# Kernel optimization log

Hardware: AMD Instinct MI355X
Metric: run time of the kernel (lower is better)

Reference implementation:

```python
import jax, jax.numpy as jnp
import numpy as np

B, T, IN = 64, 366, 24
H1, H2, HM, PEN, C = 1024, 2048, 2048, 1024, 21


def setup_inputs() -> dict:
    key = jax.random.key(0)
    ks = jax.random.split(key, 20)
    s = 0.02
    inp = {
        'x': jax.random.normal(ks[0], (B, T, IN), jnp.float32),
        'cultivar_label': jax.random.randint(ks[1], (B, 1), 0, C, jnp.int64),
        'W1': jax.random.normal(ks[2], (H1, IN), jnp.float32) * s,
        'b1': jnp.zeros((H1,), jnp.float32),
        'W2': jax.random.normal(ks[3], (H2, H1), jnp.float32) * s,
        'b2': jnp.zeros((H2,), jnp.float32),
        'W_ih': jax.random.normal(ks[4], (3 * HM, H2), jnp.float32) * s,
        'W_hh': jax.random.normal(ks[5], (3 * HM, HM), jnp.float32) * s,
        'b_ih': jnp.zeros((3 * HM,), jnp.float32),
        'b_hh': jnp.zeros((3 * HM,), jnp.float32),
        'W3': jax.random.normal(ks[6], (PEN, HM), jnp.float32) * s,
        'b3': jnp.zeros((PEN,), jnp.float32),
        'W4': jax.random.normal(ks[7], (C, PEN), jnp.float32) * s,
        'b4': jnp.zeros((C,), jnp.float32),
        'W5': jax.random.normal(ks[8], (C, PEN), jnp.float32) * s,
        'b5': jnp.zeros((C,), jnp.float32),
        'W6': jax.random.normal(ks[9], (C, PEN), jnp.float32) * s,
        'b6': jnp.zeros((C,), jnp.float32),
    }
    return inp


def _gru(x_btd, W_ih, W_hh, b_ih, b_hh):
    # PyTorch GRU, gate order (r, z, n). x_btd: [B,T,H2]
    xg = jnp.einsum('btd,gd->btg', x_btd, W_ih) + b_ih  # [B,T,3*HM]
    h0 = jnp.zeros((x_btd.shape[0], HM), x_btd.dtype)

    def step(h, xg_t):
        hg = h @ W_hh.T + b_hh
        xr, xz, xn = jnp.split(xg_t, 3, axis=-1)
        hr, hz, hn = jnp.split(hg, 3, axis=-1)
        r = jax.nn.sigmoid(xr + hr)
        z = jax.nn.sigmoid(xz + hz)
        n = jnp.tanh(xn + r * hn)
        h_new = (1.0 - z) * n + z * h
        return h_new, h_new

    h_last, hs = jax.lax.scan(step, h0, jnp.swapaxes(xg, 0, 1))
    return jnp.swapaxes(hs, 0, 1), h_last  # [B,T,HM], [B,HM]


def reference(x, cultivar_label, W1, b1, W2, b2, W_ih, W_hh, b_ih, b_hh,
              W3, b3, W4, b4, W5, b5, W6, b6):
    out = jax.nn.relu(jnp.einsum('bti,oi->bto', x, W1) + b1)
    out = jax.nn.relu(jnp.einsum('bti,oi->bto', out, W2) + b2)
    out, h_next = _gru(out, W_ih, W_hh, b_ih, b_hh)
    out_s = jax.nn.relu(jnp.einsum('bti,oi->bto', out, W3) + b3)  # [B,T,PEN]
    labels = cultivar_label[:, 0]  # [B]

    def head(W, b):
        w = W[labels]            # [B,PEN] gathered per-sample head weights
        bb = b[labels]           # [B]
        y = jnp.einsum('btp,bp->bt', out_s, w) + bb[:, None]
        return y[..., None]      # [B,T,1]

    return head(W4, b4), head(W5, b5), head(W6, b6), 0, 0
```

## Files before the change

kernel.cpp:

```cpp
#include <hip/hip_runtime.h>
#include <math.h>

#define B_   64
#define T_   366
#define IN_  24
#define H1_  1024
#define H2_  2048
#define HM_  2048
#define G3_  (3 * HM_)
#define PEN_ 1024
#define C_   21
#define BT_  (B_ * T_)

#define TC_  61
#define NCH  6
#define MC   (B_ * TC_)

typedef unsigned short bf16_t;
typedef __bf16 bf16x8 __attribute__((ext_vector_type(8)));
typedef float  f32x4  __attribute__((ext_vector_type(4)));

__device__ __forceinline__ float bf2f(bf16_t u) {
  return __uint_as_float(((unsigned int)u) << 16);
}
__device__ __forceinline__ bf16_t f2bf(float f) {
  unsigned int x = __float_as_uint(f);
  unsigned int r = (x + 0x7fffu + ((x >> 16) & 1u)) >> 16;
  return (bf16_t)r;
}

struct ushort4_t { bf16_t x, y, z, w; };

#define AS1 __attribute__((address_space(1)))
#define AS3 __attribute__((address_space(3)))

#define GBM 128
#define GBN 128
#define GBK 32
#define LDT 40

template<int WBF>
__global__ __launch_bounds__(256) void gemm_mfma(
    const bf16_t* __restrict__ A, const float* __restrict__ Wf,
    const bf16_t* __restrict__ Wb,
    const float* __restrict__ bias, bf16_t* __restrict__ C,
    int M, int N, int K, int relu)
{
  __shared__ bf16_t Asl[GBM * LDT];
  __shared__ bf16_t Wsl[GBN * LDT];
  const int tid  = threadIdx.x;
  const int m0   = blockIdx.x * GBM;
  const int n0   = blockIdx.y * GBN;
  const int wave = tid >> 6;
  const int lane = tid & 63;
  const int l16  = lane & 15;
  const int quad = lane >> 4;
  const int wm   = (wave & 1) * 64;
  const int wn   = (wave >> 1) * 64;

  f32x4 acc[4][4];
  #pragma unroll
  for (int i = 0; i < 4; ++i)
    #pragma unroll
    for (int j = 0; j < 4; ++j)
      acc[i][j] = (f32x4){0.f, 0.f, 0.f, 0.f};

  if (WBF) {
    const int r4 = lane >> 2;
    const int sg = (lane & 3) << 3;
    for (int k0 = 0; k0 < K; k0 += GBK) {
      #pragma unroll
      for (int it = 0; it < 2; ++it) {
        const int row = wave * 32 + it * 16 + r4;
        const int ar  = (m0 + row < M) ? (m0 + row) : (M - 1);
        __builtin_amdgcn_global_load_lds(
            (const AS1 void*)(A + (size_t)ar * K + k0 + sg),
            (AS3 void*)&Asl[(wave * 2 + it) * 512], 16, 0, 0);
        __builtin_amdgcn_global_load_lds(
            (const AS1 void*)(Wb + (size_t)(n0 + row) * K + k0 + sg),
            (AS3 void*)&Wsl[(wave * 2 + it) * 512], 16, 0, 0);
      }
      __syncthreads();
      bf16x8 af[4], bfr[4];
      #pragma unroll
      for (int i = 0; i < 4; ++i)
        af[i] = *(const bf16x8*)&Asl[(wm + 16 * i + l16) * 32 + quad * 8];
      #pragma unroll
      for (int j = 0; j < 4; ++j)
        bfr[j] = *(const bf16x8*)&Wsl[(wn + 16 * j + l16) * 32 + quad * 8];
      #pragma unroll
      for (int i = 0; i < 4; ++i)
        #pragma unroll
        for (int j = 0; j < 4; ++j)
          acc[i][j] = __builtin_amdgcn_mfma_f32_16x16x32_bf16(af[i], bfr[j], acc[i][j], 0, 0, 0);
      __syncthreads();
    }
  } else {
    const int srow = tid >> 1;
    const int sseg = (tid & 1) << 4;
    const int arow = (m0 + srow < M) ? (m0 + srow) : (M - 1);
    for (int k0 = 0; k0 < K; k0 += GBK) {
      {
        const bf16_t* ga = A + (size_t)arow * K + k0 + sseg;
        const uint4 a0 = *(const uint4*)ga;
        const uint4 a1 = *(const uint4*)(ga + 8);
        *(uint4*)&Asl[srow * LDT + sseg]     = a0;
        *(uint4*)&Asl[srow * LDT + sseg + 8] = a1;
        const float* gw = Wf + (size_t)(n0 + srow) * K + k0 + sseg;
        const float4 w0 = *(const float4*)gw;
        const float4 w1 = *(const float4*)(gw + 4);
        const float4 w2 = *(const float4*)(gw + 8);
        const float4 w3 = *(const float4*)(gw + 12);
        ushort4_t p0 = {f2bf(w0.x), f2bf(w0.y), f2bf(w0.z), f2bf(w0.w)};
        ushort4_t p1 = {f2bf(w1.x), f2bf(w1.y), f2bf(w1.z), f2bf(w1.w)};
        ushort4_t p2 = {f2bf(w2.x), f2bf(w2.y), f2bf(w2.z), f2bf(w2.w)};
        ushort4_t p3 = {f2bf(w3.x), f2bf(w3.y), f2bf(w3.z), f2bf(w3.w)};
        *(ushort4_t*)&Wsl[srow * LDT + sseg]      = p0;
        *(ushort4_t*)&Wsl[srow * LDT + sseg + 4]  = p1;
        *(ushort4_t*)&Wsl[srow * LDT + sseg + 8]  = p2;
        *(ushort4_t*)&Wsl[srow * LDT + sseg + 12] = p3;
      }
      __syncthreads();
      bf16x8 af[4], bfr[4];
      #pragma unroll
      for (int i = 0; i < 4; ++i)
        af[i] = *(const bf16x8*)&Asl[(wm + 16 * i + l16) * LDT + quad * 8];
      #pragma unroll
      for (int j = 0; j < 4; ++j)
        bfr[j] = *(const bf16x8*)&Wsl[(wn + 16 * j + l16) * LDT + quad * 8];
      #pragma unroll
      for (int i = 0; i < 4; ++i)
        #pragma unroll
        for (int j = 0; j < 4; ++j)
          acc[i][j] = __builtin_amdgcn_mfma_f32_16x16x32_bf16(af[i], bfr[j], acc[i][j], 0, 0, 0);
      __syncthreads();
    }
  }

  #pragma unroll
  for (int j = 0; j < 4; ++j) {
    const int n = n0 + wn + 16 * j + l16;
    const float bn = bias[n];
    #pragma unroll
    for (int i = 0; i < 4; ++i) {
      #pragma unroll
      for (int reg = 0; reg < 4; ++reg) {
        const int m = m0 + wm + 16 * i + quad * 4 + reg;
        if (m < M) {
          float v = acc[i][j][reg] + bn;
          if (relu) v = fmaxf(v, 0.f);
          C[(size_t)m * N + n] = f2bf(v);
        }
      }
    }
  }
}

#define HLD 72

__global__ __launch_bounds__(512) void gru_step(
    const bf16_t* __restrict__ h_bf_in, float* __restrict__ h_f,
    const bf16_t* __restrict__ Whh_bf, const bf16_t* __restrict__ xg_c,
    const float* __restrict__ b_hh,
    bf16_t* __restrict__ h_bf_out, bf16_t* __restrict__ hs_c, int tt)
{
  __shared__ bf16_t hst[2][2][64 * HLD];
  __shared__ bf16_t wst[2][2][48 * HLD];
  const int tid  = threadIdx.x;
  const int team = tid >> 8;
  const int ttid = tid & 255;
  const int wave = (tid >> 6) & 3;
  const int lane = tid & 63;
  const int l16  = lane & 15;
  const int quad = lane >> 4;
  const int j0   = blockIdx.x * 16;
  const int j    = j0 + l16;

  f32x4 acc[3];
  acc[0] = (f32x4){0.f, 0.f, 0.f, 0.f};
  acc[1] = acc[0];
  acc[2] = acc[0];

  const int hrow = ttid >> 2;
  const int hseg = (ttid & 3) << 4;
  const int wg   = hrow >> 4;
  const int wjr  = hrow & 15;
  const int kbase = team * (HM_ / 2);

  const bf16_t* gh_base = h_bf_in + (size_t)hrow * HM_ + kbase + hseg;
  const bf16_t* gw_base = Whh_bf + (size_t)(wg * HM_ + j0 + wjr) * HM_ + kbase + hseg;

  bf16_t xrb[4], xzb[4], xnb[4];
  float  hp[4];
  if (team == 0) {
    #pragma unroll
    for (int reg = 0; reg < 4; ++reg) {
      const int b = wave * 16 + quad * 4 + reg;
      const size_t xrow = (size_t)(b * TC_ + tt) * G3_;
      xrb[reg] = xg_c[xrow + j];
      xzb[reg] = xg_c[xrow + HM_ + j];
      xnb[reg] = xg_c[xrow + 2 * HM_ + j];
      hp[reg]  = h_f[b * HM_ + j];
    }
  }

  {
    uint4 h0 = *(const uint4*)(gh_base);
    uint4 h1 = *(const uint4*)(gh_base + 8);
    *(uint4*)&hst[team][0][hrow * HLD + hseg]     = h0;
    *(uint4*)&hst[team][0][hrow * HLD + hseg + 8] = h1;
    if (ttid < 192) {
      uint4 w0 = *(const uint4*)(gw_base);
      uint4 w1 = *(const uint4*)(gw_base + 8);
      *(uint4*)&wst[team][0][hrow * HLD + hseg]     = w0;
      *(uint4*)&wst[team][0][hrow * HLD + hseg + 8] = w1;
    }
  }
  __syncthreads();

  int cur = 0;
  for (int k0 = 0; k0 < HM_ / 2; k0 += 64) {
    uint4 nh0, nh1, nw0, nw1;
    const int have_next = (k0 + 64 < HM_ / 2);
    if (have_next) {
      nh0 = *(const uint4*)(gh_base + k0 + 64);
      nh1 = *(const uint4*)(gh_base + k0 + 64 + 8);
      if (ttid < 192) {
        nw0 = *(const uint4*)(gw_base + k0 + 64);
        nw1 = *(const uint4*)(gw_base + k0 + 64 + 8);
      }
    }
    #pragma unroll
    for (int s = 0; s < 2; ++s) {
      const bf16x8 afr = *(const bf16x8*)&hst[team][cur][(wave * 16 + l16) * HLD + s * 32 + quad * 8];
      #pragma unroll
      for (int g = 0; g < 3; ++g) {
        const bf16x8 bfr = *(const bf16x8*)&wst[team][cur][(g * 16 + l16) * HLD + s * 32 + quad * 8];
        acc[g] = __builtin_amdgcn_mfma_f32_16x16x32_bf16(afr, bfr, acc[g], 0, 0, 0);
      }
    }
    if (have_next) {
      *(uint4*)&hst[team][cur ^ 1][hrow * HLD + hseg]     = nh0;
      *(uint4*)&hst[team][cur ^ 1][hrow * HLD + hseg + 8] = nh1;
      if (ttid < 192) {
        *(uint4*)&wst[team][cur ^ 1][hrow * HLD + hseg]     = nw0;
        *(uint4*)&wst[team][cur ^ 1][hrow * HLD + hseg + 8] = nw1;
      }
    }
    __syncthreads();
    cur ^= 1;
  }

  float* red = (float*)&hst[0][0][0];
  if (team == 1) {
    #pragma unroll
    for (int g = 0; g < 3; ++g)
      #pragma unroll
      for (int r = 0; r < 4; ++r)
        red[ttid * 12 + g * 4 + r] = acc[g][r];
  }
  __syncthreads();
  if (team == 1) return;
  #pragma unroll
  for (int g = 0; g < 3; ++g)
    #pragma unroll
    for (int r = 0; r < 4; ++r)
      acc[g][r] += red[ttid * 12 + g * 4 + r];

  const float bh_r = b_hh[j];
  const float bh_z = b_hh[HM_ + j];
  const float bh_n = b_hh[2 * HM_ + j];
  #pragma unroll
  for (int reg = 0; reg < 4; ++reg) {
    const int b = wave * 16 + quad * 4 + reg;
    const float xr = bf2f(xrb[reg]);
    const float xz = bf2f(xzb[reg]);
    const float xn = bf2f(xnb[reg]);
    const float r = 1.f / (1.f + expf(-(xr + acc[0][reg] + bh_r)));
    const float z = 1.f / (1.f + expf(-(xz + acc[1][reg] + bh_z)));
    const float n = tanhf(xn + r * (acc[2][reg] + bh_n));
    const float hnew = (1.f - z) * n + z * hp[reg];
    h_f[b * HM_ + j] = hnew;
    const bf16_t hb = f2bf(hnew);
    h_bf_out[b * HM_ + j] = hb;
    hs_c[(size_t)(b * TC_ + tt) * HM_ + j] = hb;
  }
}

#define BM 64
#define BN 64
#define BKK 16

__global__ __launch_bounds__(256) void gemm_l1_gather(
    const float* __restrict__ x, const float* __restrict__ W,
    const float* __restrict__ bias, bf16_t* __restrict__ C, int t0)
{
  __shared__ float As[BKK][BM];
  __shared__ float Ws[BKK][BN];
  const int tid = threadIdx.x;
  const int m0 = blockIdx.x * BM;
  const int n0 = blockIdx.y * BN;
  const int lr = tid >> 2;
  const int kq = (tid & 3) << 2;
  const int ty = tid >> 4;
  const int tx = tid & 15;
  const int r = m0 + lr;
  const int b = r / TC_;
  const int tt = r - b * TC_;
  const size_t srow = (size_t)b * T_ + t0 + tt;
  float acc[4][4] = {};
  for (int k0 = 0; k0 < IN_; k0 += BKK) {
    {
      float v0 = 0.f, v1 = 0.f, v2 = 0.f, v3 = 0.f;
      const int kk = k0 + kq;
      const float* src = x + srow * IN_ + kk;
      if (kk + 4 <= IN_) {
        const float4 v = *(const float4*)src;
        v0 = v.x; v1 = v.y; v2 = v.z; v3 = v.w;
      }
      As[kq + 0][lr] = v0; As[kq + 1][lr] = v1;
      As[kq + 2][lr] = v2; As[kq + 3][lr] = v3;
      float w0 = 0.f, w1 = 0.f, w2 = 0.f, w3 = 0.f;
      const float* srcw = W + (size_t)(n0 + lr) * IN_ + kk;
      if (kk + 4 <= IN_) {
        const float4 w = *(const float4*)srcw;
        w0 = w.x; w1 = w.y; w2 = w.z; w3 = w.w;
      }
      Ws[kq + 0][lr] = w0; Ws[kq + 1][lr] = w1;
      Ws[kq + 2][lr] = w2; Ws[kq + 3][lr] = w3;
    }
    __syncthreads();
    #pragma unroll
    for (int k = 0; k < BKK; ++k) {
      const float4 av = *(const float4*)&As[k][ty << 2];
      const float4 bv = *(const float4*)&Ws[k][tx << 2];
      const float aa[4] = {av.x, av.y, av.z, av.w};
      const float bb[4] = {bv.x, bv.y, bv.z, bv.w};
      #pragma unroll
      for (int i = 0; i < 4; ++i)
        #pragma unroll
        for (int j = 0; j < 4; ++j)
          acc[i][j] = fmaf(aa[i], bb[j], acc[i][j]);
    }
    __syncthreads();
  }
  const float4 bvec = *(const float4*)&bias[n0 + (tx << 2)];
  const float bb[4] = {bvec.x, bvec.y, bvec.z, bvec.w};
  #pragma unroll
  for (int i = 0; i < 4; ++i) {
    ushort4_t ov;
    ov.x = f2bf(fmaxf(acc[i][0] + bb[0], 0.f));
    ov.y = f2bf(fmaxf(acc[i][1] + bb[1], 0.f));
    ov.z = f2bf(fmaxf(acc[i][2] + bb[2], 0.f));
    ov.w = f2bf(fmaxf(acc[i][3] + bb[3], 0.f));
    *(ushort4_t*)&C[(size_t)(m0 + (ty << 2) + i) * H1_ + n0 + (tx << 2)] = ov;
  }
}

__global__ __launch_bounds__(256) void heads_kernel(
    const bf16_t* __restrict__ outs_c, const int* __restrict__ label,
    const float* __restrict__ W4, const float* __restrict__ b4,
    const float* __restrict__ W5, const float* __restrict__ b5,
    const float* __restrict__ W6, const float* __restrict__ b6,
    float* __restrict__ out, int t0)
{
  const int r = blockIdx.x;
  const int b = r / TC_;
  const int tt = r - b * TC_;
  int lab = label[b];
  lab = lab < 0 ? 0 : (lab > C_ - 1 ? C_ - 1 : lab);
  const int tid = threadIdx.x;
  const bf16_t* o = outs_c + (size_t)r * PEN_;
  const float* w4 = W4 + (size_t)lab * PEN_;
  const float* w5 = W5 + (size_t)lab * PEN_;
  const float* w6 = W6 + (size_t)lab * PEN_;
  float s4 = 0.f, s5 = 0.f, s6 = 0.f;
  for (int p = tid; p < PEN_; p += 256) {
    const float ov = bf2f(o[p]);
    s4 = fmaf(ov, w4[p], s4);
    s5 = fmaf(ov, w5[p], s5);
    s6 = fmaf(ov, w6[p], s6);
  }
  #pragma unroll
  for (int off = 32; off > 0; off >>= 1) {
    s4 += __shfl_down(s4, off, 64);
    s5 += __shfl_down(s5, off, 64);
    s6 += __shfl_down(s6, off, 64);
  }
  __shared__ float red[4][3];
  const int wave = tid >> 6;
  if ((tid & 63) == 0) { red[wave][0] = s4; red[wave][1] = s5; red[wave][2] = s6; }
  __syncthreads();
  if (tid == 0) {
    const int bt = b * T_ + t0 + tt;
    out[bt]           = red[0][0] + red[1][0] + red[2][0] + red[3][0] + b4[lab];
    out[BT_ + bt]     = red[0][1] + red[1][1] + red[2][1] + red[3][1] + b5[lab];
    out[2 * BT_ + bt] = red[0][2] + red[1][2] + red[2][2] + red[3][2] + b6[lab];
    if (t0 == 0 && r == 0) { out[3 * BT_] = 0.f; out[3 * BT_ + 1] = 0.f; }
  }
}

__global__ __launch_bounds__(256) void cvt_bf(const float* __restrict__ src,
                                              bf16_t* __restrict__ dst, int n) {
  const int i = (blockIdx.x * 256 + threadIdx.x) * 4;
  if (i + 4 <= n) {
    const float4 v = *(const float4*)&src[i];
    ushort4_t o = {f2bf(v.x), f2bf(v.y), f2bf(v.z), f2bf(v.w)};
    *(ushort4_t*)&dst[i] = o;
  }
}

__global__ __launch_bounds__(256) void zero_h(float* __restrict__ hf,
                                              bf16_t* __restrict__ hb0,
                                              bf16_t* __restrict__ hb1) {
  const int i = blockIdx.x * 256 + threadIdx.x;
  hf[i] = 0.f; hb0[i] = 0; hb1[i] = 0;
}

extern "C" void kernel_launch(void* const* d_in, const int* in_sizes, int n_in,
                              void* d_out, int out_size, void* d_ws, size_t ws_size,
                              hipStream_t stream) {
  const float* x     = (const float*)d_in[0];
  const int*   label = (const int*)d_in[1];
  const float* W1    = (const float*)d_in[2];
  const float* b1    = (const float*)d_in[3];
  const float* W2    = (const float*)d_in[4];
  const float* b2    = (const float*)d_in[5];
  const float* W_ih  = (const float*)d_in[6];
  const float* W_hh  = (const float*)d_in[7];
  const float* b_ih  = (const float*)d_in[8];
  const float* b_hh  = (const float*)d_in[9];
  const float* W3    = (const float*)d_in[10];
  const float* b3    = (const float*)d_in[11];
  const float* W4    = (const float*)d_in[12];
  const float* b4    = (const float*)d_in[13];
  const float* W5    = (const float*)d_in[14];
  const float* b5    = (const float*)d_in[15];
  const float* W6    = (const float*)d_in[16];
  const float* b6    = (const float*)d_in[17];

  const size_t NEEDED  = 98172928UL;
  const size_t NEEDED2 = 131727360UL;
  if (ws_size < NEEDED) return;
  const int use_bf = (ws_size >= NEEDED2);

  char* ws = (char*)d_ws;
  bf16_t* xg_c   = (bf16_t*)(ws + 0);
  bf16_t* out2_c = (bf16_t*)(ws + 47972352UL);
  bf16_t* hs_c   = out2_c;
  bf16_t* out1_c = (bf16_t*)(ws + 63963136UL);
  bf16_t* outs_c = out1_c;
  bf16_t* Whh_bf = (bf16_t*)(ws + 71958528UL);
  float*  h_f    = (float*)(ws + 97124352UL);
  bf16_t* hbuf[2];
  hbuf[0] = (bf16_t*)(ws + 97648640UL);
  hbuf[1] = (bf16_t*)(ws + 97910784UL);
  bf16_t* W2b  = (bf16_t*)(ws + 98172928UL);
  bf16_t* Wihb = (bf16_t*)(ws + 102367232UL);
  bf16_t* W3b  = (bf16_t*)(ws + 127533056UL);
  float* out = (float*)d_out;

  const dim3 blk(256);

  cvt_bf<<<dim3(G3_ * HM_ / 1024), blk, 0, stream>>>(W_hh, Whh_bf, G3_ * HM_);
  zero_h<<<dim3(B_ * HM_ / 256), blk, 0, stream>>>(h_f, hbuf[0], hbuf[1]);
  if (use_bf) {
    cvt_bf<<<dim3(H2_ * H1_ / 1024), blk, 0, stream>>>(W2, W2b, H2_ * H1_);
    cvt_bf<<<dim3(G3_ * H2_ / 1024), blk, 0, stream>>>(W_ih, Wihb, G3_ * H2_);
    cvt_bf<<<dim3(PEN_ * HM_ / 1024), blk, 0, stream>>>(W3, W3b, PEN_ * HM_);
  }

  int pp = 0;
  for (int c = 0; c < NCH; ++c) {
    const int t0 = c * TC_;
    gemm_l1_gather<<<dim3(MC / BM, H1_ / BN), blk, 0, stream>>>(x, W1, b1, out1_c, t0);
    if (use_bf) {
      gemm_mfma<1><<<dim3((MC + GBM - 1) / GBM, H2_ / GBN), blk, 0, stream>>>(
          out1_c, nullptr, W2b, b2, out2_c, MC, H2_, H1_, 1);
      gemm_mfma<1><<<dim3((MC + GBM - 1) / GBM, G3_ / GBN), blk, 0, stream>>>(
          out2_c, nullptr, Wihb, b_ih, xg_c, MC, G3_, H2_, 0);
    } else {
      gemm_mfma<0><<<dim3((MC + GBM - 1) / GBM, H2_ / GBN), blk, 0, stream>>>(
          out1_c, W2, nullptr, b2, out2_c, MC, H2_, H1_, 1);
      gemm_mfma<0><<<dim3((MC + GBM - 1) / GBM, G3_ / GBN), blk, 0, stream>>>(
          out2_c, W_ih, nullptr, b_ih, xg_c, MC, G3_, H2_, 0);
    }

    for (int tt = 0; tt < TC_; ++tt) {
      gru_step<<<dim3(HM_ / 16), dim3(512), 0, stream>>>(
          hbuf[pp], h_f, Whh_bf, xg_c, b_hh, hbuf[1 - pp], hs_c, tt);
      pp ^= 1;
    }

    if (use_bf) {
      gemm_mfma<1><<<dim3((MC + GBM - 1) / GBM, PEN_ / GBN), blk, 0, stream>>>(
          hs_c, nullptr, W3b, b3, outs_c, MC, PEN_, HM_, 1);
    } else {
      gemm_mfma<0><<<dim3((MC + GBM - 1) / GBM, PEN_ / GBN), blk, 0, stream>>>(
          hs_c, W3, nullptr, b3, outs_c, MC, PEN_, HM_, 1);
    }
    heads_kernel<<<dim3(MC), blk, 0, stream>>>(
        outs_c, label, W4, b4, W5, b5, W6, b6, out, t0);
  }
}
```

Measured before the change: 6.945 ms.

## Split GRU recurrent GEMM K across eight waves with direct global fragment loads

The per-timestep GRU recurrent kernel no longer stages h and W_hh tiles through double-buffered shared memory in two K-halves. Each of the eight waves now covers one eighth of K, loads MFMA fragments straight from global memory (mostly L2-resident), and computes all 64 batch rows against the three gate tiles. Partial sums are reduced through shared memory, after which half the threads apply the gate nonlinearities. This drops the per-chunk barriers and LDS copies from the serial critical path. In exchange, fragment loads from global are less coalesced and the final reduction is larger.

```diff
diff --git a/kernel.cpp b/kernel.cpp
--- a/kernel.cpp
+++ b/kernel.cpp
@@ -156,43 +156,34 @@
   }
 }
 
-#define HLD 72
-
 __global__ __launch_bounds__(512) void gru_step(
     const bf16_t* __restrict__ h_bf_in, float* __restrict__ h_f,
     const bf16_t* __restrict__ Whh_bf, const bf16_t* __restrict__ xg_c,
     const float* __restrict__ b_hh,
     bf16_t* __restrict__ h_bf_out, bf16_t* __restrict__ hs_c, int tt)
 {
-  __shared__ bf16_t hst[2][2][64 * HLD];
-  __shared__ bf16_t wst[2][2][48 * HLD];
+  __shared__ float red[8][4][3][64][4];
   const int tid  = threadIdx.x;
-  const int team = tid >> 8;
-  const int ttid = tid & 255;
-  const int wave = (tid >> 6) & 3;
+  const int wv8  = tid >> 6;
   const int lane = tid & 63;
   const int l16  = lane & 15;
   const int quad = lane >> 4;
+  const int wave = wv8 & 3;
   const int j0   = blockIdx.x * 16;
   const int j    = j0 + l16;
-
-  f32x4 acc[3];
-  acc[0] = (f32x4){0.f, 0.f, 0.f, 0.f};
-  acc[1] = acc[0];
-  acc[2] = acc[0];
-
-  const int hrow = ttid >> 2;
-  const int hseg = (ttid & 3) << 4;
-  const int wg   = hrow >> 4;
-  const int wjr  = hrow & 15;
-  const int kbase = team * (HM_ / 2);
-
-  const bf16_t* gh_base = h_bf_in + (size_t)hrow * HM_ + kbase + hseg;
-  const bf16_t* gw_base = Whh_bf + (size_t)(wg * HM_ + j0 + wjr) * HM_ + kbase + hseg;
+  const int kq   = wv8 * (HM_ / 8);
+
+  const bf16_t* pa0 = h_bf_in + (size_t)(0 * 16 + l16) * HM_ + kq + quad * 8;
+  const bf16_t* pa1 = h_bf_in + (size_t)(1 * 16 + l16) * HM_ + kq + quad * 8;
+  const bf16_t* pa2 = h_bf_in + (size_t)(2 * 16 + l16) * HM_ + kq + quad * 8;
+  const bf16_t* pa3 = h_bf_in + (size_t)(3 * 16 + l16) * HM_ + kq + quad * 8;
+  const bf16_t* pb0 = Whh_bf + (size_t)(0 * HM_ + j) * HM_ + kq + quad * 8;
+  const bf16_t* pb1 = Whh_bf + (size_t)(1 * HM_ + j) * HM_ + kq + quad * 8;
+  const bf16_t* pb2 = Whh_bf + (size_t)(2 * HM_ + j) * HM_ + kq + quad * 8;
 
   bf16_t xrb[4], xzb[4], xnb[4];
   float  hp[4];
-  if (team == 0) {
+  if (tid < 256) {
     #pragma unroll
     for (int reg = 0; reg < 4; ++reg) {
       const int b = wave * 16 + quad * 4 + reg;
@@ -204,68 +195,53 @@
     }
   }
 
-  {
-    uint4 h0 = *(const uint4*)(gh_base);
-    uint4 h1 = *(const uint4*)(gh_base + 8);
-    *(uint4*)&hst[team][0][hrow * HLD + hseg]     = h0;
-    *(uint4*)&hst[team][0][hrow * HLD + hseg + 8] = h1;
-    if (ttid < 192) {
-      uint4 w0 = *(const uint4*)(gw_base);
-      uint4 w1 = *(const uint4*)(gw_base + 8);
-      *(uint4*)&wst[team][0][hrow * HLD + hseg]     = w0;
-      *(uint4*)&wst[team][0][hrow * HLD + hseg + 8] = w1;
-    }
-  }
+  f32x4 acc[4][3];
+  #pragma unroll
+  for (int rt = 0; rt < 4; ++rt)
+    #pragma unroll
+    for (int g = 0; g < 3; ++g)
+      acc[rt][g] = (f32x4){0.f, 0.f, 0.f, 0.f};
+
+  #pragma unroll
+  for (int kt = 0; kt < 8; ++kt) {
+    const int off = kt * 32;
+    const bf16x8 a0 = *(const bf16x8*)(pa0 + off);
+    const bf16x8 a1 = *(const bf16x8*)(pa1 + off);
+    const bf16x8 a2 = *(const bf16x8*)(pa2 + off);
+    const bf16x8 a3 = *(const bf16x8*)(pa3 + off);
+    const bf16x8 b0 = *(const bf16x8*)(pb0 + off);
+    const bf16x8 b1 = *(const bf16x8*)(pb1 + off);
+    const bf16x8 b2 = *(const bf16x8*)(pb2 + off);
+    acc[0][0] = __builtin_amdgcn_mfma_f32_16x16x32_bf16(a0, b0, acc[0][0], 0, 0, 0);
+    acc[0][1] = __builtin_amdgcn_mfma_f32_16x16x32_bf16(a0, b1, acc[0][1], 0, 0, 0);
+    acc[0][2] = __builtin_amdgcn_mfma_f32_16x16x32_bf16(a0, b2, acc[0][2], 0, 0, 0);
+    acc[1][0] = __builtin_amdgcn_mfma_f32_16x16x32_bf16(a1, b0, acc[1][0], 0, 0, 0);
+    acc[1][1] = __builtin_amdgcn_mfma_f32_16x16x32_bf16(a1, b1, acc[1][1], 0, 0, 0);
+    acc[1][2] = __builtin_amdgcn_mfma_f32_16x16x32_bf16(a1, b2, acc[1][2], 0, 0, 0);
+    acc[2][0] = __builtin_amdgcn_mfma_f32_16x16x32_bf16(a2, b0, acc[2][0], 0, 0, 0);
+    acc[2][1] = __builtin_amdgcn_mfma_f32_16x16x32_bf16(a2, b1, acc[2][1], 0, 0, 0);
+    acc[2][2] = __builtin_amdgcn_mfma_f32_16x16x32_bf16(a2, b2, acc[2][2], 0, 0, 0);
+    acc[3][0] = __builtin_amdgcn_mfma_f32_16x16x32_bf16(a3, b0, acc[3][0], 0, 0, 0);
+    acc[3][1] = __builtin_amdgcn_mfma_f32_16x16x32_bf16(a3, b1, acc[3][1], 0, 0, 0);
+    acc[3][2] = __builtin_amdgcn_mfma_f32_16x16x32_bf16(a3, b2, acc[3][2], 0, 0, 0);
+  }
+
+  #pragma unroll
+  for (int rt = 0; rt < 4; ++rt)
+    #pragma unroll
+    for (int g = 0; g < 3; ++g)
+      *(f32x4*)&red[wv8][rt][g][lane][0] = acc[rt][g];
   __syncthreads();
-
-  int cur = 0;
-  for (int k0 = 0; k0 < HM_ / 2; k0 += 64) {
-    uint4 nh0, nh1, nw0, nw1;
-    const int have_next = (k0 + 64 < HM_ / 2);
-    if (have_next) {
-      nh0 = *(const uint4*)(gh_base + k0 + 64);
-      nh1 = *(const uint4*)(gh_base + k0 + 64 + 8);
-      if (ttid < 192) {
-        nw0 = *(const uint4*)(gw_base + k0 + 64);
-        nw1 = *(const uint4*)(gw_base + k0 + 64 + 8);
-      }
-    }
-    #pragma unroll
-    for (int s = 0; s < 2; ++s) {
-      const bf16x8 afr = *(const bf16x8*)&hst[team][cur][(wave * 16 + l16) * HLD + s * 32 + quad * 8];
-      #pragma unroll
-      for (int g = 0; g < 3; ++g) {
-        const bf16x8 bfr = *(const bf16x8*)&wst[team][cur][(g * 16 + l16) * HLD + s * 32 + quad * 8];
-        acc[g] = __builtin_amdgcn_mfma_f32_16x16x32_bf16(afr, bfr, acc[g], 0, 0, 0);
-      }
-    }
-    if (have_next) {
-      *(uint4*)&hst[team][cur ^ 1][hrow * HLD + hseg]     = nh0;
-      *(uint4*)&hst[team][cur ^ 1][hrow * HLD + hseg + 8] = nh1;
-      if (ttid < 192) {
-        *(uint4*)&wst[team][cur ^ 1][hrow * HLD + hseg]     = nw0;
-        *(uint4*)&wst[team][cur ^ 1][hrow * HLD + hseg + 8] = nw1;
-      }
-    }
-    __syncthreads();
-    cur ^= 1;
-  }
-
-  float* red = (float*)&hst[0][0][0];
-  if (team == 1) {
-    #pragma unroll
-    for (int g = 0; g < 3; ++g)
-      #pragma unroll
-      for (int r = 0; r < 4; ++r)
-        red[ttid * 12 + g * 4 + r] = acc[g][r];
-  }
-  __syncthreads();
-  if (team == 1) return;
-  #pragma unroll
-  for (int g = 0; g < 3; ++g)
-    #pragma unroll
-    for (int r = 0; r < 4; ++r)
-      acc[g][r] += red[ttid * 12 + g * 4 + r];
+  if (tid >= 256) return;
+
+  f32x4 s0 = (f32x4){0.f, 0.f, 0.f, 0.f};
+  f32x4 s1 = s0, s2 = s0;
+  #pragma unroll
+  for (int wv = 0; wv < 8; ++wv) {
+    s0 += *(const f32x4*)&red[wv][wave][0][lane][0];
+    s1 += *(const f32x4*)&red[wv][wave][1][lane][0];
+    s2 += *(const f32x4*)&red[wv][wave][2][lane][0];
+  }
 
   const float bh_r = b_hh[j];
   const float bh_z = b_hh[HM_ + j];
@@ -276,9 +252,9 @@
     const float xr = bf2f(xrb[reg]);
     const float xz = bf2f(xzb[reg]);
     const float xn = bf2f(xnb[reg]);
-    const float r = 1.f / (1.f + expf(-(xr + acc[0][reg] + bh_r)));
-    const float z = 1.f / (1.f + expf(-(xz + acc[1][reg] + bh_z)));
-    const float n = tanhf(xn + r * (acc[2][reg] + bh_n));
+    const float r = 1.f / (1.f + expf(-(xr + s0[reg] + bh_r)));
+    const float z = 1.f / (1.f + expf(-(xz + s1[reg] + bh_z)));
+    const float n = tanhf(xn + r * (s2[reg] + bh_n));
     const float hnew = (1.f - z) * n + z * hp[reg];
     h_f[b * HM_ + j] = hnew;
     const bf16_t hb = f2bf(hnew);
```

Result: slower. 7.673 ms (+10.5%).

## Halve GRU step block width to 8 hidden units to double grid parallelism

Applied to the files above, without the earlier changes.

Each GRU step block now covers 8 hidden columns instead of 16, so the launch grid doubles to 256 blocks and fills more compute units. The three gate slices are packed into two 16x16 MFMA tiles, using 24 weight rows per k-slice instead of 48. The elementwise gate update is spread across all 512 threads through a shared-memory transpose. The explicit LDS double buffer is replaced by a single buffer with two barriers per k-iteration. The cost is half-wasted MFMA work on the second tile, the h tile being reloaded by twice as many blocks, and extra synchronisation.

```diff
diff --git a/kernel.cpp b/kernel.cpp
--- a/kernel.cpp
+++ b/kernel.cpp
@@ -164,126 +164,111 @@
     const float* __restrict__ b_hh,
     bf16_t* __restrict__ h_bf_out, bf16_t* __restrict__ hs_c, int tt)
 {
-  __shared__ bf16_t hst[2][2][64 * HLD];
-  __shared__ bf16_t wst[2][2][48 * HLD];
+  __shared__ char smem[25344];
+  bf16_t* hst = (bf16_t*)smem;
+  bf16_t* wst = (bf16_t*)(smem + 18432);
+  float*  red = (float*)smem;
+  float*  sm_g = (float*)(smem + 18432);
+
   const int tid  = threadIdx.x;
   const int team = tid >> 8;
   const int ttid = tid & 255;
-  const int wave = (tid >> 6) & 3;
+  const int w4   = (tid >> 6) & 3;
   const int lane = tid & 63;
   const int l16  = lane & 15;
   const int quad = lane >> 4;
-  const int j0   = blockIdx.x * 16;
-  const int j    = j0 + l16;
-
-  f32x4 acc[3];
-  acc[0] = (f32x4){0.f, 0.f, 0.f, 0.f};
-  acc[1] = acc[0];
-  acc[2] = acc[0];
+  const int j0   = blockIdx.x * 8;
+  const int kbase = team * (HM_ / 2);
+
+  f32x4 acc0 = (f32x4){0.f, 0.f, 0.f, 0.f};
+  f32x4 acc1 = acc0;
 
   const int hrow = ttid >> 2;
   const int hseg = (ttid & 3) << 4;
-  const int wg   = hrow >> 4;
-  const int wjr  = hrow & 15;
-  const int kbase = team * (HM_ / 2);
+  const int wrow = ttid >> 3;
+  const int wgi  = wrow >> 3;
+  const int wjr  = wrow & 7;
+  const int wseg = (ttid & 7) << 3;
 
   const bf16_t* gh_base = h_bf_in + (size_t)hrow * HM_ + kbase + hseg;
-  const bf16_t* gw_base = Whh_bf + (size_t)(wg * HM_ + j0 + wjr) * HM_ + kbase + hseg;
-
-  bf16_t xrb[4], xzb[4], xnb[4];
-  float  hp[4];
+  const bf16_t* gw_base = Whh_bf + (size_t)(wgi * HM_ + j0 + wjr) * HM_ + kbase + wseg;
+
+  const int ej  = tid & 7;
+  const int eb  = tid >> 3;
+  const int jje = j0 + ej;
+  const size_t xrow = (size_t)(eb * TC_ + tt) * G3_;
+  const bf16_t xrb = xg_c[xrow + jje];
+  const bf16_t xzb = xg_c[xrow + HM_ + jje];
+  const bf16_t xnb = xg_c[xrow + 2 * HM_ + jje];
+  const float  hp  = h_f[eb * HM_ + jje];
+  const float bh_r = b_hh[jje];
+  const float bh_z = b_hh[HM_ + jje];
+  const float bh_n = b_hh[2 * HM_ + jje];
+
+  uint4 h0 = *(const uint4*)(gh_base);
+  uint4 h1 = *(const uint4*)(gh_base + 8);
+  uint4 w0 = {0u,0u,0u,0u};
+  if (ttid < 192) w0 = *(const uint4*)(gw_base);
+
+  bf16_t* hT = hst + team * (64 * HLD);
+  bf16_t* wT = wst + team * (24 * HLD);
+
+  for (int k0 = 0; k0 < HM_ / 2; k0 += 64) {
+    *(uint4*)&hT[hrow * HLD + hseg]     = h0;
+    *(uint4*)&hT[hrow * HLD + hseg + 8] = h1;
+    if (ttid < 192) *(uint4*)&wT[wrow * HLD + wseg] = w0;
+    __syncthreads();
+    if (k0 + 64 < HM_ / 2) {
+      h0 = *(const uint4*)(gh_base + k0 + 64);
+      h1 = *(const uint4*)(gh_base + k0 + 64 + 8);
+      if (ttid < 192) w0 = *(const uint4*)(gw_base + k0 + 64);
+    }
+    #pragma unroll
+    for (int s = 0; s < 2; ++s) {
+      const bf16x8 afr = *(const bf16x8*)&hT[(w4 * 16 + l16) * HLD + s * 32 + quad * 8];
+      const bf16x8 b0t = *(const bf16x8*)&wT[l16 * HLD + s * 32 + quad * 8];
+      const bf16x8 b1t = *(const bf16x8*)&wT[(16 + (l16 & 7)) * HLD + s * 32 + quad * 8];
+      acc0 = __builtin_amdgcn_mfma_f32_16x16x32_bf16(afr, b0t, acc0, 0, 0, 0);
+      acc1 = __builtin_amdgcn_mfma_f32_16x16x32_bf16(afr, b1t, acc1, 0, 0, 0);
+    }
+    __syncthreads();
+  }
+
+  if (team == 1) {
+    *(f32x4*)&red[((w4 * 2 + 0) * 64 + lane) * 4] = acc0;
+    *(f32x4*)&red[((w4 * 2 + 1) * 64 + lane) * 4] = acc1;
+  }
+  __syncthreads();
+
   if (team == 0) {
+    const f32x4 t1a = *(const f32x4*)&red[((w4 * 2 + 0) * 64 + lane) * 4];
+    const f32x4 t1b = *(const f32x4*)&red[((w4 * 2 + 1) * 64 + lane) * 4];
+    const f32x4 s0 = acc0 + t1a;
+    const f32x4 s1 = acc1 + t1b;
+    const int ga = (l16 < 8) ? 0 : 1;
+    const int jja = l16 & 7;
     #pragma unroll
     for (int reg = 0; reg < 4; ++reg) {
-      const int b = wave * 16 + quad * 4 + reg;
-      const size_t xrow = (size_t)(b * TC_ + tt) * G3_;
-      xrb[reg] = xg_c[xrow + j];
-      xzb[reg] = xg_c[xrow + HM_ + j];
-      xnb[reg] = xg_c[xrow + 2 * HM_ + j];
-      hp[reg]  = h_f[b * HM_ + j];
-    }
-  }
+      const int b = w4 * 16 + quad * 4 + reg;
+      sm_g[(ga * 8 + jja) * 64 + b] = s0[reg];
+      if (l16 < 8) sm_g[(2 * 8 + l16) * 64 + b] = s1[reg];
+    }
+  }
+  __syncthreads();
 
   {
-    uint4 h0 = *(const uint4*)(gh_base);
-    uint4 h1 = *(const uint4*)(gh_base + 8);
-    *(uint4*)&hst[team][0][hrow * HLD + hseg]     = h0;
-    *(uint4*)&hst[team][0][hrow * HLD + hseg + 8] = h1;
-    if (ttid < 192) {
-      uint4 w0 = *(const uint4*)(gw_base);
-      uint4 w1 = *(const uint4*)(gw_base + 8);
-      *(uint4*)&wst[team][0][hrow * HLD + hseg]     = w0;
-      *(uint4*)&wst[team][0][hrow * HLD + hseg + 8] = w1;
-    }
-  }
-  __syncthreads();
-
-  int cur = 0;
-  for (int k0 = 0; k0 < HM_ / 2; k0 += 64) {
-    uint4 nh0, nh1, nw0, nw1;
-    const int have_next = (k0 + 64 < HM_ / 2);
-    if (have_next) {
-      nh0 = *(const uint4*)(gh_base + k0 + 64);
-      nh1 = *(const uint4*)(gh_base + k0 + 64 + 8);
-      if (ttid < 192) {
-        nw0 = *(const uint4*)(gw_base + k0 + 64);
-        nw1 = *(const uint4*)(gw_base + k0 + 64 + 8);
-      }
-    }
-    #pragma unroll
-    for (int s = 0; s < 2; ++s) {
-      const bf16x8 afr = *(const bf16x8*)&hst[team][cur][(wave * 16 + l16) * HLD + s * 32 + quad * 8];
-      #pragma unroll
-      for (int g = 0; g < 3; ++g) {
-        const bf16x8 bfr = *(const bf16x8*)&wst[team][cur][(g * 16 + l16) * HLD + s * 32 + quad * 8];
-        acc[g] = __builtin_amdgcn_mfma_f32_16x16x32_bf16(afr, bfr, acc[g], 0, 0, 0);
-      }
-    }
-    if (have_next) {
-      *(uint4*)&hst[team][cur ^ 1][hrow * HLD + hseg]     = nh0;
-      *(uint4*)&hst[team][cur ^ 1][hrow * HLD + hseg + 8] = nh1;
-      if (ttid < 192) {
-        *(uint4*)&wst[team][cur ^ 1][hrow * HLD + hseg]     = nw0;
-        *(uint4*)&wst[team][cur ^ 1][hrow * HLD + hseg + 8] = nw1;
-      }
-    }
-    __syncthreads();
-    cur ^= 1;
-  }
-
-  float* red = (float*)&hst[0][0][0];
-  if (team == 1) {
-    #pragma unroll
-    for (int g = 0; g < 3; ++g)
-      #pragma unroll
-      for (int r = 0; r < 4; ++r)
-        red[ttid * 12 + g * 4 + r] = acc[g][r];
-  }
-  __syncthreads();
-  if (team == 1) return;
-  #pragma unroll
-  for (int g = 0; g < 3; ++g)
-    #pragma unroll
-    for (int r = 0; r < 4; ++r)
-      acc[g][r] += red[ttid * 12 + g * 4 + r];
-
-  const float bh_r = b_hh[j];
-  const float bh_z = b_hh[HM_ + j];
-  const float bh_n = b_hh[2 * HM_ + j];
-  #pragma unroll
-  for (int reg = 0; reg < 4; ++reg) {
-    const int b = wave * 16 + quad * 4 + reg;
-    const float xr = bf2f(xrb[reg]);
-    const float xz = bf2f(xzb[reg]);
-    const float xn = bf2f(xnb[reg]);
-    const float r = 1.f / (1.f + expf(-(xr + acc[0][reg] + bh_r)));
-    const float z = 1.f / (1.f + expf(-(xz + acc[1][reg] + bh_z)));
-    const float n = tanhf(xn + r * (acc[2][reg] + bh_n));
-    const float hnew = (1.f - z) * n + z * hp[reg];
-    h_f[b * HM_ + j] = hnew;
+    const float sr = sm_g[(0 * 8 + ej) * 64 + eb];
+    const float sz = sm_g[(1 * 8 + ej) * 64 + eb];
+    const float sn = sm_g[(2 * 8 + ej) * 64 + eb];
+    const float xr = bf2f(xrb), xz = bf2f(xzb), xn = bf2f(xnb);
+    const float r = 1.f / (1.f + expf(-(xr + sr + bh_r)));
+    const float z = 1.f / (1.f + expf(-(xz + sz + bh_z)));
+    const float n = tanhf(xn + r * (sn + bh_n));
+    const float hnew = (1.f - z) * n + z * hp;
+    h_f[eb * HM_ + jje] = hnew;
     const bf16_t hb = f2bf(hnew);
-    h_bf_out[b * HM_ + j] = hb;
-    hs_c[(size_t)(b * TC_ + tt) * HM_ + j] = hb;
+    h_bf_out[eb * HM_ + jje] = hb;
+    hs_c[(size_t)(eb * TC_ + tt) * HM_ + jje] = hb;
   }
 }
 
@@ -487,7 +472,7 @@
     }
 
     for (int tt = 0; tt < TC_; ++tt) {
-      gru_step<<<dim3(HM_ / 16), dim3(512), 0, stream>>>(
+      gru_step<<<dim3(HM_ / 8), dim3(512), 0, stream>>>(
           hbuf[pp], h_f, Whh_bf, xg_c, b_hh, hbuf[1 - pp], hs_c, tt);
       pp ^= 1;
     }
```

After: 6.656 ms. 4.2% less time.
